# Kernel optimization log

Measured on AMD Instinct MI355X. Metric: run time of the kernel, lower is better.

The kernel has to match this reference:

```python
import jax, jax.numpy as jnp
import numpy as np

B, S, D_IN, D_OUT, W = 32, 4096, 512, 300, 1024
S_INNER = S - 2
EPS = 1e-5


def _make_spans(rng):
    """Build ragged word spans (contiguous, variable length) padded to W."""
    starts = np.zeros((B, W), dtype=np.int32)
    ends = np.ones((B, W), dtype=np.int32)  # padded spans are (0,1); masked + zeroed later
    mask = np.ones((B, W), dtype=bool)
    for b in range(B):
        n = int(rng.integers(W // 2, W + 1))
        lens = rng.integers(1, 5, size=n)
        e = np.cumsum(lens)
        e = e[e <= S_INNER]
        n = len(e)
        s = e - lens[:n]
        starts[b, :n] = s
        ends[b, :n] = e
        mask[b, :n] = False
    return starts, ends, mask


def setup_inputs() -> dict:
    key = jax.random.key(0)
    k1, k2, k3, k4, k5, k6, k7 = jax.random.split(key, 7)
    rng = np.random.default_rng(0)
    starts, ends, mask = _make_spans(rng)
    return {
        "t_lhs": jax.random.normal(k1, (B, S, D_IN), dtype=jnp.float32),
        "W_lin": jax.random.normal(k2, (D_OUT, D_IN), dtype=jnp.float32) / np.sqrt(D_IN),
        "b_lin": jax.random.normal(k3, (D_OUT,), dtype=jnp.float32) * 0.01,
        "gamma": jnp.ones((D_OUT,), dtype=jnp.float32),
        "beta": jnp.zeros((D_OUT,), dtype=jnp.float32),
        "w_score": jax.random.normal(k4, (1, D_OUT), dtype=jnp.float32) / np.sqrt(D_OUT),
        "b_score": jax.random.normal(k5, (1,), dtype=jnp.float32) * 0.01,
        "word_starts": jnp.asarray(starts),
        "word_ends": jnp.asarray(ends),
        "key_padding_mask": jnp.asarray(mask),
        "lam": 1,
    }


def reference(t_lhs, W_lin, b_lin, gamma, beta, w_score, b_score,
              word_starts, word_ends, key_padding_mask, lam):
    tt = t_lhs[:, 1:-1, :]                                   # [B, S-2, D_in]
    # Contiguous-span mean via exclusive cumsum: mean = (csum[e]-csum[s])/(e-s)
    csum = jnp.concatenate([jnp.zeros_like(tt[:, :1]), jnp.cumsum(tt, axis=1)], axis=1)  # [B, S-1, D_in]
    gs = jnp.take_along_axis(csum, word_starts[:, :, None], axis=1)  # [B, W, D_in]
    ge = jnp.take_along_axis(csum, word_ends[:, :, None], axis=1)
    cnt = (word_ends - word_starts).astype(tt.dtype)[:, :, None]
    means = (ge - gs) / jnp.maximum(cnt, 1.0)
    # pad_sequence zero-pads beyond each batch's word count
    ttt = jnp.where(key_padding_mask[:, :, None], 0.0, means)        # [B, W, D_in]
    # Linear 512->300 then LayerNorm(300)
    x = jnp.einsum('bwd,od->bwo', ttt, W_lin) + b_lin                # [B, W, D_out]
    mu = jnp.mean(x, axis=-1, keepdims=True)
    var = jnp.mean(jnp.square(x - mu), axis=-1, keepdims=True)
    text_output = (x - mu) / jnp.sqrt(var + EPS) * gamma + beta
    # score: Linear 300->1, masked softmax over word dim
    score = jnp.einsum('bwo,o->bw', text_output, w_score[0]) + b_score[0]
    score = jnp.where(key_padding_mask, -jnp.inf, score) * lam
    probs = jax.nn.softmax(score, axis=1)                            # [B, W]
    text_score = jnp.broadcast_to(probs[:, :, None], text_output.shape)  # repeat over D_out
    return (text_output, text_score)
```

## Files before the change

### kernel.cpp

```cpp
#include <hip/hip_runtime.h>
#include <hip/hip_bf16.h>

#define NB 32
#define NS 4096
#define DIN 512
#define DOUT 300
#define NPAD 304
#define NW 1024
#define NTILE 19
#define EPSF 1e-5f

typedef __attribute__((ext_vector_type(8))) short bf16x8;
typedef __attribute__((ext_vector_type(4))) float f32x4;

__device__ __forceinline__ unsigned short f2bf(float f) {
    unsigned int u = __float_as_uint(f);
    unsigned int r = (u + 0x7FFFu + ((u >> 16) & 1u)) >> 16;
    return (unsigned short)r;
}

__device__ __forceinline__ bool word_valid(int e, int w) { return e > w; }

__global__ void k_prep(const float* __restrict__ W_lin, const float* __restrict__ b_lin,
                       unsigned short* __restrict__ Wl, float* __restrict__ bpad) {
    int o = blockIdx.x, t = threadIdx.x;
    for (int k = t; k < DIN; k += 128) {
        float v = (o < DOUT) ? W_lin[o * DIN + k] : 0.f;
        Wl[o * DIN + k] = f2bf(v);
    }
    if (t == 0) bpad[o] = (o < DOUT) ? b_lin[o] : 0.f;
}

__global__ __launch_bounds__(256) void k_spanmean(
    const float* __restrict__ t_lhs, const int* __restrict__ starts,
    const int* __restrict__ ends, unsigned short* __restrict__ A) {
    int wave = blockIdx.x * 4 + (threadIdx.x >> 6);
    int lane = threadIdx.x & 63;
    for (int word = wave; word < NB * NW; word += 8192) {
        int b = word >> 10;
        int w = word & (NW - 1);
        int s = starts[word];
        int e = ends[word];
        float4 a0 = make_float4(0.f, 0.f, 0.f, 0.f);
        float4 a1 = make_float4(0.f, 0.f, 0.f, 0.f);
        if (word_valid(e, w)) {
            const float* base = t_lhs + ((size_t)b * NS + 1 + s) * DIN + lane * 8;
            int cnt = e - s;
            for (int r = 0; r < cnt; ++r) {
                float4 v0 = *reinterpret_cast<const float4*>(base + (size_t)r * DIN);
                float4 v1 = *reinterpret_cast<const float4*>(base + (size_t)r * DIN + 4);
                a0.x += v0.x; a0.y += v0.y; a0.z += v0.z; a0.w += v0.w;
                a1.x += v1.x; a1.y += v1.y; a1.z += v1.z; a1.w += v1.w;
            }
            float inv = 1.f / (float)cnt;
            a0.x *= inv; a0.y *= inv; a0.z *= inv; a0.w *= inv;
            a1.x *= inv; a1.y *= inv; a1.z *= inv; a1.w *= inv;
        }
        uint4 o;
        o.x = (unsigned)f2bf(a0.x) | ((unsigned)f2bf(a0.y) << 16);
        o.y = (unsigned)f2bf(a0.z) | ((unsigned)f2bf(a0.w) << 16);
        o.z = (unsigned)f2bf(a1.x) | ((unsigned)f2bf(a1.y) << 16);
        o.w = (unsigned)f2bf(a1.z) | ((unsigned)f2bf(a1.w) << 16);
        *reinterpret_cast<uint4*>(A + (size_t)word * DIN + lane * 8) = o;
    }
}

__global__ __launch_bounds__(256) void k_gemm_ln(
    const unsigned short* __restrict__ A, const unsigned short* __restrict__ Wl,
    const float* __restrict__ bpad, const float* __restrict__ gamma,
    const float* __restrict__ beta, const float* __restrict__ w_score,
    const float* __restrict__ b_score, float* __restrict__ out0,
    float* __restrict__ score) {
    int wid = threadIdx.x >> 6, lane = threadIdx.x & 63;
    int lr = lane & 15, kg = lane >> 4;
    size_t rowBase = (size_t)blockIdx.x * 64 + (size_t)wid * 16;

    f32x4 acc[NTILE];
#pragma unroll
    for (int i = 0; i < NTILE; ++i) acc[i] = (f32x4){0.f, 0.f, 0.f, 0.f};

    const short* Ap = reinterpret_cast<const short*>(A) + (rowBase + lr) * DIN + kg * 8;
    const short* Bp = reinterpret_cast<const short*>(Wl) + (size_t)lr * DIN + kg * 8;

    for (int kt = 0; kt < DIN; kt += 32) {
        bf16x8 av = *reinterpret_cast<const bf16x8*>(Ap + kt);
#pragma unroll
        for (int nt = 0; nt < NTILE; ++nt) {
            bf16x8 bv = *reinterpret_cast<const bf16x8*>(Bp + (size_t)nt * 16 * DIN + kt);
            acc[nt] = __builtin_amdgcn_mfma_f32_16x16x32_bf16(av, bv, acc[nt], 0, 0, 0);
        }
    }

    float s[4] = {0, 0, 0, 0}, q[4] = {0, 0, 0, 0};
#pragma unroll
    for (int nt = 0; nt < NTILE; ++nt) {
        float bias = bpad[nt * 16 + lr];
#pragma unroll
        for (int r = 0; r < 4; ++r) {
            float v = acc[nt][r] + bias;
            acc[nt][r] = v;
            s[r] += v; q[r] += v * v;
        }
    }
#pragma unroll
    for (int m = 1; m <= 8; m <<= 1) {
#pragma unroll
        for (int r = 0; r < 4; ++r) {
            s[r] += __shfl_xor(s[r], m);
            q[r] += __shfl_xor(q[r], m);
        }
    }
    float mu[4], rstd[4];
#pragma unroll
    for (int r = 0; r < 4; ++r) {
        mu[r] = s[r] * (1.f / DOUT);
        float var = q[r] * (1.f / DOUT) - mu[r] * mu[r];
        rstd[r] = rsqrtf(var + EPSF);
    }
    float sc[4] = {0, 0, 0, 0};
#pragma unroll
    for (int nt = 0; nt < NTILE; ++nt) {
        int col = nt * 16 + lr;
        bool cv = (col < DOUT);
        float g = cv ? gamma[col] : 0.f;
        float bb = cv ? beta[col] : 0.f;
        float wv = cv ? w_score[col] : 0.f;
#pragma unroll
        for (int r = 0; r < 4; ++r) {
            float y = (acc[nt][r] - mu[r]) * rstd[r] * g + bb;
            if (cv) out0[(rowBase + kg * 4 + r) * DOUT + col] = y;
            sc[r] += y * wv;
        }
    }
#pragma unroll
    for (int m = 1; m <= 8; m <<= 1) {
#pragma unroll
        for (int r = 0; r < 4; ++r) sc[r] += __shfl_xor(sc[r], m);
    }
    if (lr == 0) {
        float bs = b_score[0];
#pragma unroll
        for (int r = 0; r < 4; ++r) score[rowBase + kg * 4 + r] = sc[r] + bs;
    }
}

__global__ void k_softmax(const float* __restrict__ score, const int* __restrict__ ends,
                          const int* __restrict__ lam, float* __restrict__ probs) {
    __shared__ float red[16];
    int b = blockIdx.x, w = threadIdx.x;
    bool valid = word_valid(ends[b * NW + w], w);
    float lamf = (float)lam[0];
    float scv = valid ? score[b * NW + w] * lamf : -INFINITY;
    float m = scv;
#pragma unroll
    for (int d = 1; d <= 32; d <<= 1) m = fmaxf(m, __shfl_xor(m, d));
    int wid = w >> 6, lane = w & 63;
    if (lane == 0) red[wid] = m;
    __syncthreads();
    float mx = -INFINITY;
#pragma unroll
    for (int i = 0; i < 16; ++i) mx = fmaxf(mx, red[i]);
    __syncthreads();
    float e = valid ? expf(scv - mx) : 0.f;
    float su = e;
#pragma unroll
    for (int d = 1; d <= 32; d <<= 1) su += __shfl_xor(su, d);
    if (lane == 0) red[wid] = su;
    __syncthreads();
    float tot = 0.f;
#pragma unroll
    for (int i = 0; i < 16; ++i) tot += red[i];
    probs[b * NW + w] = e / tot;
}

__global__ __launch_bounds__(256) void k_bcast(const float* __restrict__ probs,
                                               float* __restrict__ out1) {
    unsigned idx = blockIdx.x * 256 + threadIdx.x;
#pragma unroll
    for (int it = 0; it < 4; ++it) {
        unsigned word = (unsigned)(((unsigned long long)idx * 458129845ULL) >> 35);
        unsigned r = idx - word * 75u;
        float p = probs[word];
        float4 v = make_float4(p, p, p, p);
        reinterpret_cast<float4*>(out1)[(size_t)word * 75 + r] = v;
        idx += 614400u;
    }
}

extern "C" void kernel_launch(void* const* d_in, const int* in_sizes, int n_in,
                              void* d_out, int out_size, void* d_ws, size_t ws_size,
                              hipStream_t stream) {
    const float* t_lhs   = (const float*)d_in[0];
    const float* W_lin   = (const float*)d_in[1];
    const float* b_lin   = (const float*)d_in[2];
    const float* gamma   = (const float*)d_in[3];
    const float* beta    = (const float*)d_in[4];
    const float* w_score = (const float*)d_in[5];
    const float* b_score = (const float*)d_in[6];
    const int*   starts  = (const int*)d_in[7];
    const int*   ends    = (const int*)d_in[8];
    const int*   lam     = (const int*)d_in[10];

    float* out0 = (float*)d_out;
    float* out1 = out0 + (size_t)NB * NW * DOUT;

    const size_t A_bytes = (size_t)NB * NW * DIN * 2;
    char* ws = (char*)d_ws;
    size_t off = 0;
    unsigned short* Wl = (unsigned short*)(ws + off); off += (size_t)NPAD * DIN * 2;
    float* bpad  = (float*)(ws + off); off += 1536;
    float* score = (float*)(ws + off); off += (size_t)NB * NW * 4;
    float* probs = (float*)(ws + off); off += (size_t)NB * NW * 4;
    unsigned short* A;
    if (ws_size >= off + A_bytes) {
        A = (unsigned short*)(ws + off);
    } else {
        A = (unsigned short*)out1;
    }

    hipLaunchKernelGGL(k_prep,     dim3(NPAD), dim3(128), 0, stream, W_lin, b_lin, Wl, bpad);
    hipLaunchKernelGGL(k_spanmean, dim3(2048), dim3(256), 0, stream, t_lhs, starts, ends, A);
    hipLaunchKernelGGL(k_gemm_ln,  dim3(NB * NW / 64), dim3(256), 0, stream, A, Wl, bpad, gamma, beta,
                       w_score, b_score, out0, score);
    hipLaunchKernelGGL(k_softmax,  dim3(NB),   dim3(NW),  0, stream, score, ends, lam, probs);
    hipLaunchKernelGGL(k_bcast,    dim3(2400), dim3(256), 0, stream, probs, out1);
}
```

Baseline: 498.3 us.

## Fuse all stages into one cooperative persistent kernel with LDS-staged span means

Replaces five kernel launches with a single cooperative kernel that uses grid-wide syncs between the weight prep, fused span-mean+GEMM+LayerNorm, softmax and broadcast phases. The span means for each 64-row tile are now written to shared memory and consumed directly by the MFMA GEMM, so the bf16 intermediate A never goes through global memory. This removes launch gaps and the A round trip, but grid size is capped at 512 blocks with at most 2 per CU, which limits latency hiding for the gather loads. Softmax runs on only 32 blocks while the rest idle at the grid barrier.

```diff
diff --git a/kernel.cpp b/kernel.cpp
--- a/kernel.cpp
+++ b/kernel.cpp
@@ -1,5 +1,8 @@
 #include <hip/hip_runtime.h>
+#include <hip/hip_cooperative_groups.h>
 #include <hip/hip_bf16.h>
+
+namespace cg = cooperative_groups;
 
 #define NB 32
 #define NS 4096
@@ -9,181 +12,183 @@
 #define NW 1024
 #define NTILE 19
 #define EPSF 1e-5f
+#define WTILES 512
+#define LDSROW 520
 
 typedef __attribute__((ext_vector_type(8))) short bf16x8;
 typedef __attribute__((ext_vector_type(4))) float f32x4;
 
 __device__ __forceinline__ unsigned short f2bf(float f) {
     unsigned int u = __float_as_uint(f);
-    unsigned int r = (u + 0x7FFFu + ((u >> 16) & 1u)) >> 16;
-    return (unsigned short)r;
+    return (unsigned short)((u + 0x7FFFu + ((u >> 16) & 1u)) >> 16);
 }
 
 __device__ __forceinline__ bool word_valid(int e, int w) { return e > w; }
 
-__global__ void k_prep(const float* __restrict__ W_lin, const float* __restrict__ b_lin,
-                       unsigned short* __restrict__ Wl, float* __restrict__ bpad) {
-    int o = blockIdx.x, t = threadIdx.x;
-    for (int k = t; k < DIN; k += 128) {
-        float v = (o < DOUT) ? W_lin[o * DIN + k] : 0.f;
-        Wl[o * DIN + k] = f2bf(v);
+__global__ __launch_bounds__(256, 2) void k_all(
+    const float* __restrict__ t_lhs, const float* __restrict__ W_lin,
+    const float* __restrict__ b_lin, const float* __restrict__ gamma,
+    const float* __restrict__ beta, const float* __restrict__ w_score,
+    const float* __restrict__ b_score, const int* __restrict__ starts,
+    const int* __restrict__ ends, const int* __restrict__ lam,
+    float* __restrict__ out0, float* __restrict__ out1,
+    unsigned short* __restrict__ Wl, float* __restrict__ bpad,
+    float* __restrict__ score, float* __restrict__ probs)
+{
+    __shared__ unsigned short Asm[64][LDSROW];
+    __shared__ float red[4];
+    cg::grid_group grid = cg::this_grid();
+    const int tid = threadIdx.x, bid = blockIdx.x;
+    const int nblk = gridDim.x, gsz = nblk * 256;
+    const int gid = bid * 256 + tid;
+    const int wave = tid >> 6, lane = tid & 63;
+    const int lr = lane & 15, kg = lane >> 4;
+
+    for (int i = gid; i < NPAD * DIN; i += gsz)
+        Wl[i] = f2bf(i < DOUT * DIN ? W_lin[i] : 0.f);
+    for (int i = gid; i < NPAD; i += gsz)
+        bpad[i] = (i < DOUT) ? b_lin[i] : 0.f;
+    grid.sync();
+
+    for (int wb = bid; wb < WTILES; wb += nblk) {
+        for (int j = 0; j < 16; ++j) {
+            int lw = wave * 16 + j;
+            int word = wb * 64 + lw;
+            int w = word & (NW - 1);
+            int s = starts[word], e = ends[word];
+            float4 a0 = make_float4(0.f, 0.f, 0.f, 0.f);
+            float4 a1 = make_float4(0.f, 0.f, 0.f, 0.f);
+            if (word_valid(e, w)) {
+                const float* base = t_lhs + ((size_t)(word >> 10) * NS + 1 + s) * DIN + lane * 8;
+                int cnt = e - s;
+                for (int r = 0; r < cnt; ++r) {
+                    float4 v0 = *reinterpret_cast<const float4*>(base + (size_t)r * DIN);
+                    float4 v1 = *reinterpret_cast<const float4*>(base + (size_t)r * DIN + 4);
+                    a0.x += v0.x; a0.y += v0.y; a0.z += v0.z; a0.w += v0.w;
+                    a1.x += v1.x; a1.y += v1.y; a1.z += v1.z; a1.w += v1.w;
+                }
+                float inv = 1.f / (float)cnt;
+                a0.x *= inv; a0.y *= inv; a0.z *= inv; a0.w *= inv;
+                a1.x *= inv; a1.y *= inv; a1.z *= inv; a1.w *= inv;
+            }
+            uint4 o;
+            o.x = (unsigned)f2bf(a0.x) | ((unsigned)f2bf(a0.y) << 16);
+            o.y = (unsigned)f2bf(a0.z) | ((unsigned)f2bf(a0.w) << 16);
+            o.z = (unsigned)f2bf(a1.x) | ((unsigned)f2bf(a1.y) << 16);
+            o.w = (unsigned)f2bf(a1.z) | ((unsigned)f2bf(a1.w) << 16);
+            *reinterpret_cast<uint4*>(&Asm[lw][lane * 8]) = o;
+        }
+        __syncthreads();
+
+        f32x4 acc[NTILE];
+#pragma unroll
+        for (int i = 0; i < NTILE; ++i) acc[i] = (f32x4){0.f, 0.f, 0.f, 0.f};
+        const short* Bp = reinterpret_cast<const short*>(Wl) + (size_t)lr * DIN + kg * 8;
+        const int arow = wave * 16 + lr;
+        for (int kt = 0; kt < DIN; kt += 32) {
+            bf16x8 av = *reinterpret_cast<const bf16x8*>(&Asm[arow][kt + kg * 8]);
+#pragma unroll
+            for (int nt = 0; nt < NTILE; ++nt) {
+                bf16x8 bv = *reinterpret_cast<const bf16x8*>(Bp + (size_t)nt * 16 * DIN + kt);
+                acc[nt] = __builtin_amdgcn_mfma_f32_16x16x32_bf16(av, bv, acc[nt], 0, 0, 0);
+            }
+        }
+
+        size_t rowBase = (size_t)wb * 64 + wave * 16;
+        float s4[4] = {0, 0, 0, 0}, q4[4] = {0, 0, 0, 0};
+#pragma unroll
+        for (int nt = 0; nt < NTILE; ++nt) {
+            float bias = bpad[nt * 16 + lr];
+#pragma unroll
+            for (int r = 0; r < 4; ++r) {
+                float v = acc[nt][r] + bias;
+                acc[nt][r] = v;
+                s4[r] += v; q4[r] += v * v;
+            }
+        }
+#pragma unroll
+        for (int m = 1; m <= 8; m <<= 1) {
+#pragma unroll
+            for (int r = 0; r < 4; ++r) {
+                s4[r] += __shfl_xor(s4[r], m);
+                q4[r] += __shfl_xor(q4[r], m);
+            }
+        }
+        float mu[4], rstd[4];
+#pragma unroll
+        for (int r = 0; r < 4; ++r) {
+            mu[r] = s4[r] * (1.f / DOUT);
+            float var = q4[r] * (1.f / DOUT) - mu[r] * mu[r];
+            rstd[r] = rsqrtf(var + EPSF);
+        }
+        float sc[4] = {0, 0, 0, 0};
+#pragma unroll
+        for (int nt = 0; nt < NTILE; ++nt) {
+            int col = nt * 16 + lr;
+            bool cv = (col < DOUT);
+            float g = cv ? gamma[col] : 0.f;
+            float bb = cv ? beta[col] : 0.f;
+            float wv = cv ? w_score[col] : 0.f;
+#pragma unroll
+            for (int r = 0; r < 4; ++r) {
+                float y = (acc[nt][r] - mu[r]) * rstd[r] * g + bb;
+                if (cv) out0[(rowBase + kg * 4 + r) * DOUT + col] = y;
+                sc[r] += y * wv;
+            }
+        }
+#pragma unroll
+        for (int m = 1; m <= 8; m <<= 1) {
+#pragma unroll
+            for (int r = 0; r < 4; ++r) sc[r] += __shfl_xor(sc[r], m);
+        }
+        if (lr == 0) {
+            float bs = b_score[0];
+#pragma unroll
+            for (int r = 0; r < 4; ++r) score[rowBase + kg * 4 + r] = sc[r] + bs;
+        }
+        __syncthreads();
     }
-    if (t == 0) bpad[o] = (o < DOUT) ? b_lin[o] : 0.f;
-}
-
-__global__ __launch_bounds__(256) void k_spanmean(
-    const float* __restrict__ t_lhs, const int* __restrict__ starts,
-    const int* __restrict__ ends, unsigned short* __restrict__ A) {
-    int wave = blockIdx.x * 4 + (threadIdx.x >> 6);
-    int lane = threadIdx.x & 63;
-    for (int word = wave; word < NB * NW; word += 8192) {
-        int b = word >> 10;
-        int w = word & (NW - 1);
-        int s = starts[word];
-        int e = ends[word];
-        float4 a0 = make_float4(0.f, 0.f, 0.f, 0.f);
-        float4 a1 = make_float4(0.f, 0.f, 0.f, 0.f);
-        if (word_valid(e, w)) {
-            const float* base = t_lhs + ((size_t)b * NS + 1 + s) * DIN + lane * 8;
-            int cnt = e - s;
-            for (int r = 0; r < cnt; ++r) {
-                float4 v0 = *reinterpret_cast<const float4*>(base + (size_t)r * DIN);
-                float4 v1 = *reinterpret_cast<const float4*>(base + (size_t)r * DIN + 4);
-                a0.x += v0.x; a0.y += v0.y; a0.z += v0.z; a0.w += v0.w;
-                a1.x += v1.x; a1.y += v1.y; a1.z += v1.z; a1.w += v1.w;
-            }
-            float inv = 1.f / (float)cnt;
-            a0.x *= inv; a0.y *= inv; a0.z *= inv; a0.w *= inv;
-            a1.x *= inv; a1.y *= inv; a1.z *= inv; a1.w *= inv;
-        }
-        uint4 o;
-        o.x = (unsigned)f2bf(a0.x) | ((unsigned)f2bf(a0.y) << 16);
-        o.y = (unsigned)f2bf(a0.z) | ((unsigned)f2bf(a0.w) << 16);
-        o.z = (unsigned)f2bf(a1.x) | ((unsigned)f2bf(a1.y) << 16);
-        o.w = (unsigned)f2bf(a1.z) | ((unsigned)f2bf(a1.w) << 16);
-        *reinterpret_cast<uint4*>(A + (size_t)word * DIN + lane * 8) = o;
+    __threadfence();
+    grid.sync();
+
+    for (int b = bid; b < NB; b += nblk) {
+        float lamf = (float)lam[0];
+        float sv[4], ev[4];
+        bool vld[4];
+        float mloc = -INFINITY;
+#pragma unroll
+        for (int j = 0; j < 4; ++j) {
+            int w = tid + 256 * j;
+            bool v = word_valid(ends[b * NW + w], w);
+            float x = v ? score[b * NW + w] * lamf : -INFINITY;
+            vld[j] = v; sv[j] = x;
+            mloc = fmaxf(mloc, x);
+        }
+#pragma unroll
+        for (int d = 1; d <= 32; d <<= 1) mloc = fmaxf(mloc, __shfl_xor(mloc, d));
+        if (lane == 0) red[wave] = mloc;
+        __syncthreads();
+        float mx = fmaxf(fmaxf(red[0], red[1]), fmaxf(red[2], red[3]));
+        __syncthreads();
+        float sloc = 0.f;
+#pragma unroll
+        for (int j = 0; j < 4; ++j) { ev[j] = vld[j] ? expf(sv[j] - mx) : 0.f; sloc += ev[j]; }
+#pragma unroll
+        for (int d = 1; d <= 32; d <<= 1) sloc += __shfl_xor(sloc, d);
+        if (lane == 0) red[wave] = sloc;
+        __syncthreads();
+        float tot = red[0] + red[1] + red[2] + red[3];
+#pragma unroll
+        for (int j = 0; j < 4; ++j) probs[b * NW + tid + 256 * j] = ev[j] / tot;
+        __syncthreads();
     }
-}
-
-__global__ __launch_bounds__(256) void k_gemm_ln(
-    const unsigned short* __restrict__ A, const unsigned short* __restrict__ Wl,
-    const float* __restrict__ bpad, const float* __restrict__ gamma,
-    const float* __restrict__ beta, const float* __restrict__ w_score,
-    const float* __restrict__ b_score, float* __restrict__ out0,
-    float* __restrict__ score) {
-    int wid = threadIdx.x >> 6, lane = threadIdx.x & 63;
-    int lr = lane & 15, kg = lane >> 4;
-    size_t rowBase = (size_t)blockIdx.x * 64 + (size_t)wid * 16;
-
-    f32x4 acc[NTILE];
-#pragma unroll
-    for (int i = 0; i < NTILE; ++i) acc[i] = (f32x4){0.f, 0.f, 0.f, 0.f};
-
-    const short* Ap = reinterpret_cast<const short*>(A) + (rowBase + lr) * DIN + kg * 8;
-    const short* Bp = reinterpret_cast<const short*>(Wl) + (size_t)lr * DIN + kg * 8;
-
-    for (int kt = 0; kt < DIN; kt += 32) {
-        bf16x8 av = *reinterpret_cast<const bf16x8*>(Ap + kt);
-#pragma unroll
-        for (int nt = 0; nt < NTILE; ++nt) {
-            bf16x8 bv = *reinterpret_cast<const bf16x8*>(Bp + (size_t)nt * 16 * DIN + kt);
-            acc[nt] = __builtin_amdgcn_mfma_f32_16x16x32_bf16(av, bv, acc[nt], 0, 0, 0);
-        }
-    }
-
-    float s[4] = {0, 0, 0, 0}, q[4] = {0, 0, 0, 0};
-#pragma unroll
-    for (int nt = 0; nt < NTILE; ++nt) {
-        float bias = bpad[nt * 16 + lr];
-#pragma unroll
-        for (int r = 0; r < 4; ++r) {
-            float v = acc[nt][r] + bias;
-            acc[nt][r] = v;
-            s[r] += v; q[r] += v * v;
-        }
-    }
-#pragma unroll
-    for (int m = 1; m <= 8; m <<= 1) {
-#pragma unroll
-        for (int r = 0; r < 4; ++r) {
-            s[r] += __shfl_xor(s[r], m);
-            q[r] += __shfl_xor(q[r], m);
-        }
-    }
-    float mu[4], rstd[4];
-#pragma unroll
-    for (int r = 0; r < 4; ++r) {
-        mu[r] = s[r] * (1.f / DOUT);
-        float var = q[r] * (1.f / DOUT) - mu[r] * mu[r];
-        rstd[r] = rsqrtf(var + EPSF);
-    }
-    float sc[4] = {0, 0, 0, 0};
-#pragma unroll
-    for (int nt = 0; nt < NTILE; ++nt) {
-        int col = nt * 16 + lr;
-        bool cv = (col < DOUT);
-        float g = cv ? gamma[col] : 0.f;
-        float bb = cv ? beta[col] : 0.f;
-        float wv = cv ? w_score[col] : 0.f;
-#pragma unroll
-        for (int r = 0; r < 4; ++r) {
-            float y = (acc[nt][r] - mu[r]) * rstd[r] * g + bb;
-            if (cv) out0[(rowBase + kg * 4 + r) * DOUT + col] = y;
-            sc[r] += y * wv;
-        }
-    }
-#pragma unroll
-    for (int m = 1; m <= 8; m <<= 1) {
-#pragma unroll
-        for (int r = 0; r < 4; ++r) sc[r] += __shfl_xor(sc[r], m);
-    }
-    if (lr == 0) {
-        float bs = b_score[0];
-#pragma unroll
-        for (int r = 0; r < 4; ++r) score[rowBase + kg * 4 + r] = sc[r] + bs;
-    }
-}
-
-__global__ void k_softmax(const float* __restrict__ score, const int* __restrict__ ends,
-                          const int* __restrict__ lam, float* __restrict__ probs) {
-    __shared__ float red[16];
-    int b = blockIdx.x, w = threadIdx.x;
-    bool valid = word_valid(ends[b * NW + w], w);
-    float lamf = (float)lam[0];
-    float scv = valid ? score[b * NW + w] * lamf : -INFINITY;
-    float m = scv;
-#pragma unroll
-    for (int d = 1; d <= 32; d <<= 1) m = fmaxf(m, __shfl_xor(m, d));
-    int wid = w >> 6, lane = w & 63;
-    if (lane == 0) red[wid] = m;
-    __syncthreads();
-    float mx = -INFINITY;
-#pragma unroll
-    for (int i = 0; i < 16; ++i) mx = fmaxf(mx, red[i]);
-    __syncthreads();
-    float e = valid ? expf(scv - mx) : 0.f;
-    float su = e;
-#pragma unroll
-    for (int d = 1; d <= 32; d <<= 1) su += __shfl_xor(su, d);
-    if (lane == 0) red[wid] = su;
-    __syncthreads();
-    float tot = 0.f;
-#pragma unroll
-    for (int i = 0; i < 16; ++i) tot += red[i];
-    probs[b * NW + w] = e / tot;
-}
-
-__global__ __launch_bounds__(256) void k_bcast(const float* __restrict__ probs,
-                                               float* __restrict__ out1) {
-    unsigned idx = blockIdx.x * 256 + threadIdx.x;
-#pragma unroll
-    for (int it = 0; it < 4; ++it) {
-        unsigned word = (unsigned)(((unsigned long long)idx * 458129845ULL) >> 35);
-        unsigned r = idx - word * 75u;
+    __threadfence();
+    grid.sync();
+
+    for (unsigned i = gid; i < 2457600u; i += (unsigned)gsz) {
+        unsigned word = (unsigned)(((unsigned long long)i * 458129845ULL) >> 35);
         float p = probs[word];
-        float4 v = make_float4(p, p, p, p);
-        reinterpret_cast<float4*>(out1)[(size_t)word * 75 + r] = v;
-        idx += 614400u;
+        reinterpret_cast<float4*>(out1)[i] = make_float4(p, p, p, p);
     }
 }
 
@@ -204,24 +209,26 @@
     float* out0 = (float*)d_out;
     float* out1 = out0 + (size_t)NB * NW * DOUT;
 
-    const size_t A_bytes = (size_t)NB * NW * DIN * 2;
     char* ws = (char*)d_ws;
-    size_t off = 0;
-    unsigned short* Wl = (unsigned short*)(ws + off); off += (size_t)NPAD * DIN * 2;
-    float* bpad  = (float*)(ws + off); off += 1536;
-    float* score = (float*)(ws + off); off += (size_t)NB * NW * 4;
-    float* probs = (float*)(ws + off); off += (size_t)NB * NW * 4;
-    unsigned short* A;
-    if (ws_size >= off + A_bytes) {
-        A = (unsigned short*)(ws + off);
-    } else {
-        A = (unsigned short*)out1;
-    }
-
-    hipLaunchKernelGGL(k_prep,     dim3(NPAD), dim3(128), 0, stream, W_lin, b_lin, Wl, bpad);
-    hipLaunchKernelGGL(k_spanmean, dim3(2048), dim3(256), 0, stream, t_lhs, starts, ends, A);
-    hipLaunchKernelGGL(k_gemm_ln,  dim3(NB * NW / 64), dim3(256), 0, stream, A, Wl, bpad, gamma, beta,
-                       w_score, b_score, out0, score);
-    hipLaunchKernelGGL(k_softmax,  dim3(NB),   dim3(NW),  0, stream, score, ends, lam, probs);
-    hipLaunchKernelGGL(k_bcast,    dim3(2400), dim3(256), 0, stream, probs, out1);
+    unsigned short* Wl = (unsigned short*)ws;
+    float* bpad  = (float*)(ws + 311296);
+    float* score = (float*)(ws + 312576);
+    float* probs = (float*)(ws + 443648);
+
+    int dev = 0;
+    hipGetDevice(&dev);
+    int nCU = 256;
+    hipDeviceGetAttribute(&nCU, hipDeviceAttributeMultiprocessorCount, dev);
+    int maxPerCU = 0;
+    hipOccupancyMaxActiveBlocksPerMultiprocessor(&maxPerCU, k_all, 256, 0);
+    if (maxPerCU < 1) maxPerCU = 1;
+    int nblk = nCU * maxPerCU;
+    if (nblk > WTILES) nblk = WTILES;
+
+    void* args[] = {
+        (void*)&t_lhs, (void*)&W_lin, (void*)&b_lin, (void*)&gamma, (void*)&beta,
+        (void*)&w_score, (void*)&b_score, (void*)&starts, (void*)&ends, (void*)&lam,
+        (void*)&out0, (void*)&out1, (void*)&Wl, (void*)&bpad, (void*)&score, (void*)&probs
+    };
+    hipLaunchCooperativeKernel((const void*)k_all, dim3(nblk), dim3(256), args, 0, stream);
 }
```

New measurement: 799.0 us. 60.3% more time.
